# Performance work log

Measured on AMD Instinct MI355X. Metric: run time of the kernel, lower is better.

## Reference

```python
import jax, jax.numpy as jnp
import numpy as np

TOP_K = 2


def setup_inputs() -> dict:
    key = jax.random.key(0)
    ks = jax.random.split(key, 5)
    B, S, H, F, E = 1, 2048, 1024, 3584, 8
    scale_h = 1.0 / np.sqrt(H)
    scale_f = 1.0 / np.sqrt(F)
    return {
        "hidden_states": jax.random.normal(ks[0], (B, S, H), dtype=jnp.float32),
        "gate_w": jax.random.normal(ks[1], (E, H), dtype=jnp.float32) * scale_h,
        "w1": jax.random.normal(ks[2], (E, H, F), dtype=jnp.float32) * scale_h,
        "w3": jax.random.normal(ks[3], (E, H, F), dtype=jnp.float32) * scale_h,
        "w2": jax.random.normal(ks[4], (E, F, H), dtype=jnp.float32) * scale_f,
    }


def reference(hidden_states, gate_w, w1, w2, w3):
    B, S, H = hidden_states.shape
    E = gate_w.shape[0]
    x = hidden_states.reshape(-1, H)  # [T, H]
    # Router: logits -> fp32 softmax -> top-k -> renormalize
    router_logits = x @ gate_w.T  # [T, E]
    probs = jax.nn.softmax(router_logits.astype(jnp.float32), axis=-1)
    top_w, top_idx = jax.lax.top_k(probs, TOP_K)  # [T, K]
    top_w = top_w / jnp.sum(top_w, axis=-1, keepdims=True)
    top_w = top_w.astype(x.dtype)
    # Dense combine weights [T, E]: routing weight if expert selected else 0
    combine = jnp.sum(jax.nn.one_hot(top_idx, E, dtype=x.dtype) * top_w[..., None], axis=1)
    # Per-expert SwiGLU FFN, weighted-summed (loop over small fixed E)
    out = jnp.zeros_like(x)
    for e in range(E):
        h = jax.nn.silu(x @ w1[e]) * (x @ w3[e])  # [T, F]
        out = out + (h @ w2[e]) * combine[:, e:e + 1]
    return out.reshape(B, S, H), router_logits
```

## Files before the change

kernel.cpp:

```cpp
#include <hip/hip_runtime.h>
#include <cstdint>
#include <cstddef>

#define Tt 2048
#define Hh 1024
#define Ff 3584
#define Ee 8
#define ROWS_CAP 5120
#define MAXT 40

#define OFF_CTRL   0u
#define OFF_TOKE   4096u
#define OFF_TOKW   (4096u + 16384u)
#define OFF_ROWMAP 65536u
#define OFF_ROWW   98304u
#define OFF_XG     262144ull
#define OFF_G      10747904ull
#define OFF_W1T    47448064ull
#define OFF_W3T    106168320ull
#define OFF_W2T    164888576ull

typedef __attribute__((ext_vector_type(8))) short bf16x8;
typedef __attribute__((ext_vector_type(4))) float f32x4;

__device__ __forceinline__ unsigned short f2bf(float f) {
  unsigned int u = __float_as_uint(f);
  u += 0x7fffu + ((u >> 16) & 1u);
  return (unsigned short)(u >> 16);
}

__device__ __forceinline__ unsigned pkbf(float a, float b) {
  unsigned r;
  asm("v_cvt_pk_bf16_f32 %0, %1, %2" : "=v"(r) : "v"(a), "v"(b));
  return r;
}

__device__ __forceinline__ void gload_lds16(const void* g, void* l) {
  auto gp = (const __attribute__((address_space(1))) char*)(uintptr_t)g;
  auto lp = (__attribute__((address_space(3))) char*)(uintptr_t)l;
  __builtin_amdgcn_global_load_lds(gp, lp, 16, 0, 0);
}

__device__ __forceinline__ bf16x8 frg(const char* lds, int row, int gc) {
  return *(const bf16x8*)(lds + row * 64 + ((gc ^ ((row >> 1) & 3)) * 16));
}

__device__ __forceinline__ void tc_tile(const float* __restrict__ src,
                                        unsigned short* __restrict__ dst,
                                        int R, int C, int r0g, int c0,
                                        char* sT, int t) {
  const int col4 = (t & 15) * 4, rb = (t >> 4) * 8;
  float4 v[8];
#pragma unroll
  for (int i = 0; i < 8; ++i)
    v[i] = *(const float4*)(src + (size_t)(r0g + rb + i) * C + c0 + col4);
#pragma unroll
  for (int j = 0; j < 4; ++j) {
    int c = col4 + j;
    int M = (((c & 7) ^ ((c >> 3) & 7)) << 4);
    uint4 q;
    q.x = pkbf(((const float*)&v[0])[j], ((const float*)&v[1])[j]);
    q.y = pkbf(((const float*)&v[2])[j], ((const float*)&v[3])[j]);
    q.z = pkbf(((const float*)&v[4])[j], ((const float*)&v[5])[j]);
    q.w = pkbf(((const float*)&v[6])[j], ((const float*)&v[7])[j]);
    *(uint4*)(sT + c * 256 + ((rb * 2) ^ M)) = q;
  }
  __syncthreads();
  const int oc = t >> 2, part = t & 3;
  const int M = (((oc & 7) ^ ((oc >> 3) & 7)) << 4);
#pragma unroll
  for (int i = 0; i < 4; ++i) {
    uint4 q = *(const uint4*)(sT + oc * 256 + ((i * 64 + part * 16) ^ M));
    *(uint4*)(dst + (size_t)(c0 + oc) * R + r0g + i * 32 + part * 8) = q;
  }
}

__global__ __launch_bounds__(256) void router_tc1(
    const float* __restrict__ x, const float* __restrict__ gw,
    float* __restrict__ logits_out, int* __restrict__ tok_e,
    float* __restrict__ tok_w, int* __restrict__ ctrl,
    const float* __restrict__ w1, unsigned short* __restrict__ w1T) {
  __shared__ alignas(16) char sT[16384];
  if (blockIdx.x >= 512) {
    int b = blockIdx.x - 512;
    int e = b / 448, rem = b % 448;
    int tr = rem / 56, tcc = rem % 56;
    tc_tile(w1 + (size_t)e * Hh * Ff, w1T + (size_t)e * Hh * Ff,
            Hh, Ff, tr * 128, tcc * 64, sT, threadIdx.x);
    return;
  }
  const int lane = threadIdx.x & 63;
  const int t = blockIdx.x * 4 + (threadIdx.x >> 6);
  const float4* xp = (const float4*)(x + (size_t)t * Hh + lane * 16);
  float4 x0 = xp[0], x1 = xp[1], x2 = xp[2], x3 = xp[3];
  float lg[Ee];
#pragma unroll
  for (int e = 0; e < Ee; ++e) {
    const float4* gp = (const float4*)(gw + e * Hh + lane * 16);
    float4 g0 = gp[0], g1 = gp[1], g2 = gp[2], g3 = gp[3];
    float s = x0.x*g0.x + x0.y*g0.y + x0.z*g0.z + x0.w*g0.w
            + x1.x*g1.x + x1.y*g1.y + x1.z*g1.z + x1.w*g1.w
            + x2.x*g2.x + x2.y*g2.y + x2.z*g2.z + x2.w*g2.w
            + x3.x*g3.x + x3.y*g3.y + x3.z*g3.z + x3.w*g3.w;
#pragma unroll
    for (int o = 32; o; o >>= 1) s += __shfl_xor(s, o);
    lg[e] = s;
  }
  if (lane == 0) {
    float m = lg[0];
#pragma unroll
    for (int e = 1; e < Ee; ++e) m = fmaxf(m, lg[e]);
    float p[Ee];
#pragma unroll
    for (int e = 0; e < Ee; ++e) p[e] = expf(lg[e] - m);
    int a0 = 0;
#pragma unroll
    for (int e = 1; e < Ee; ++e) if (p[e] > p[a0]) a0 = e;
    int a1 = (a0 == 0) ? 1 : 0;
#pragma unroll
    for (int e = 0; e < Ee; ++e) if (e != a0 && p[e] > p[a1]) a1 = e;
    float rs = p[a0] + p[a1];
    float w0 = p[a0] / rs, w1v = p[a1] / rs;
#pragma unroll
    for (int e = 0; e < Ee; ++e) logits_out[(size_t)t * Ee + e] = lg[e];
    tok_e[t * 2] = a0; tok_e[t * 2 + 1] = a1;
    tok_w[t * 2] = w0; tok_w[t * 2 + 1] = w1v;
    atomicAdd(&ctrl[a0], 1); atomicAdd(&ctrl[a1], 1);
  }
}

__global__ void offsets_kernel(int* ctrl) {
  if (threadIdx.x == 0) {
    int acc = 0;
    for (int e = 0; e < Ee; ++e) {
      ctrl[16 + e] = acc;
      acc += ((ctrl[e] + 127) >> 7) << 7;
    }
    ctrl[16 + Ee] = acc;
    int idx = 0;
    for (int e = 0; e < Ee; ++e) {
      int nt = (ctrl[e] + 127) >> 7;
      for (int m = 0; m < nt && idx < MAXT; ++m) {
        ctrl[32 + 2 * idx] = e;
        ctrl[33 + 2 * idx] = ctrl[16 + e] + m * 128;
        ++idx;
      }
    }
    for (; idx < MAXT; ++idx) { ctrl[32 + 2 * idx] = 0; ctrl[33 + 2 * idx] = -1; }
  }
}

__global__ __launch_bounds__(512) void assign_kernel(
    int* ctrl, const int* __restrict__ tok_e, const float* __restrict__ tok_w,
    int* __restrict__ rowmap, float* __restrict__ roww) {
  int i = blockIdx.x * 512 + threadIdx.x;
  if (i < 2 * Tt) {
    int e = tok_e[i];
    int pos = atomicAdd(&ctrl[8 + e], 1);
    int r = ctrl[16 + e] + pos;
    rowmap[r] = i >> 1;
    roww[r] = tok_w[i];
  }
  if (i < Ee * 128) {
    int e = i >> 7, pd = i & 127;
    int o = ctrl[16 + e], o1 = ctrl[16 + e + 1], c = ctrl[e];
    int r = o + c + pd;
    if (r < o1) { rowmap[r] = -1; roww[r] = 0.f; }
  }
}

__global__ __launch_bounds__(256) void gather_tc3(
    const float* __restrict__ x, const int* __restrict__ ctrl,
    const int* __restrict__ rowmap, unsigned short* __restrict__ Xg,
    const float* __restrict__ w3, unsigned short* __restrict__ w3T) {
  __shared__ alignas(16) char sT[16384];
  if (blockIdx.x >= 2560) {
    int b = blockIdx.x - 2560;
    int e = b / 448, rem = b % 448;
    int tr = rem / 56, tcc = rem % 56;
    tc_tile(w3 + (size_t)e * Hh * Ff, w3T + (size_t)e * Hh * Ff,
            Hh, Ff, tr * 128, tcc * 64, sT, threadIdx.x);
    return;
  }
  int r = blockIdx.x * 2 + (threadIdx.x >> 7);
  int j = threadIdx.x & 127;
  if (r >= ctrl[16 + Ee]) return;
  int t = rowmap[r];
  uint4 v = make_uint4(0u, 0u, 0u, 0u);
  if (t >= 0) {
    const float4* xp = (const float4*)(x + (size_t)t * Hh + j * 8);
    float4 a = xp[0], b = xp[1];
    v.x = (unsigned)f2bf(a.x) | ((unsigned)f2bf(a.y) << 16);
    v.y = (unsigned)f2bf(a.z) | ((unsigned)f2bf(a.w) << 16);
    v.z = (unsigned)f2bf(b.x) | ((unsigned)f2bf(b.y) << 16);
    v.w = (unsigned)f2bf(b.z) | ((unsigned)f2bf(b.w) << 16);
  }
  *(uint4*)(Xg + (size_t)r * Hh + j * 8) = v;
}

__global__ __launch_bounds__(512, 4) void h13_tc2(
    const unsigned short* __restrict__ Xg, const unsigned short* __restrict__ w1T,
    const unsigned short* __restrict__ w3T, const int* __restrict__ ctrl,
    unsigned short* __restrict__ G,
    const float* __restrict__ w2, unsigned short* __restrict__ w2T) {
  __shared__ alignas(16) char sLDS[49152];
  int lin = blockIdx.y * 28 + blockIdx.x;
  if (lin >= 1120) {
    int idx = lin - 1120;
    int s = threadIdx.x >> 8;
    int tile = idx * 2 + s;
    int e = tile / 448, rem = tile % 448;
    int tr = rem / 16, tcc = rem % 16;
    tc_tile(w2 + (size_t)e * Ff * Hh, w2T + (size_t)e * Ff * Hh,
            Ff, Hh, tr * 128, tcc * 64, sLDS + s * 16384, threadIdx.x & 255);
    return;
  }
  char* sA  = sLDS;
  char* sB1 = sLDS + 16384;
  char* sB3 = sLDS + 32768;
  int wg = (lin & 7) * 140 + (lin >> 3);
  int ft = wg % 40, bx = wg / 40;
  const int e = ctrl[32 + 2 * ft];
  const int row0 = ctrl[33 + 2 * ft];
  if (row0 < 0) return;
  const int n0 = bx * 128;
  const int tid = threadIdx.x, lane = tid & 63, wv = tid >> 6;
  const int wr = wv >> 2, wc = wv & 3;
  const unsigned short* w1e = w1T + (size_t)e * Ff * Hh;
  const unsigned short* w3e = w3T + (size_t)e * Ff * Hh;
  f32x4 acc1[4][2] = {};
  f32x4 acc3[4][2] = {};
  const int srow = wv * 16 + (lane >> 2);
  const int sgc = (lane & 3) ^ ((lane >> 3) & 3);
  const unsigned short* gA  = Xg  + (size_t)(row0 + srow) * Hh + sgc * 8;
  const unsigned short* gB1 = w1e + (size_t)(n0 + srow) * Hh + sgc * 8;
  const unsigned short* gB3 = w3e + (size_t)(n0 + srow) * Hh + sgc * 8;

  gload_lds16(gA,  sA  + wv * 1024);
  gload_lds16(gB1, sB1 + wv * 1024);
  gload_lds16(gB3, sB3 + wv * 1024);
  __syncthreads();

  for (int it = 0; it < 32; ++it) {
    const int cur = it & 1;
    if (it < 31) {
      const size_t ko = (size_t)(it + 1) * 32;
      gload_lds16(gA + ko,  sA  + (cur ^ 1) * 8192 + wv * 1024);
      gload_lds16(gB1 + ko, sB1 + (cur ^ 1) * 8192 + wv * 1024);
      gload_lds16(gB3 + ko, sB3 + (cur ^ 1) * 8192 + wv * 1024);
    }
    const int gc = lane >> 4;
    bf16x8 af[4];
#pragma unroll
    for (int mi = 0; mi < 4; ++mi)
      af[mi] = frg(sA + cur * 8192, wr * 64 + mi * 16 + (lane & 15), gc);
    __builtin_amdgcn_s_setprio(1);
#pragma unroll
    for (int ni = 0; ni < 2; ++ni) {
      bf16x8 b1 = frg(sB1 + cur * 8192, wc * 32 + ni * 16 + (lane & 15), gc);
      bf16x8 b3 = frg(sB3 + cur * 8192, wc * 32 + ni * 16 + (lane & 15), gc);
#pragma unroll
      for (int mi = 0; mi < 4; ++mi) {
        acc1[mi][ni] = __builtin_amdgcn_mfma_f32_16x16x32_bf16(af[mi], b1, acc1[mi][ni], 0, 0, 0);
        acc3[mi][ni] = __builtin_amdgcn_mfma_f32_16x16x32_bf16(af[mi], b3, acc3[mi][ni], 0, 0, 0);
      }
    }
    __builtin_amdgcn_s_setprio(0);
    __syncthreads();
  }
  const int rb = wr * 64 + 4 * (lane >> 4), cb = wc * 32 + (lane & 15);
#pragma unroll
  for (int mi = 0; mi < 4; ++mi)
#pragma unroll
    for (int ni = 0; ni < 2; ++ni)
#pragma unroll
      for (int r = 0; r < 4; ++r) {
        float h1 = acc1[mi][ni][r], h3 = acc3[mi][ni][r];
        float gv = h1 / (1.f + __expf(-h1)) * h3;
        G[(size_t)(row0 + rb + mi * 16 + r) * Ff + n0 + cb + ni * 16] = f2bf(gv);
      }
}

__global__ __launch_bounds__(512, 4) void ffn2_gemm(
    const unsigned short* __restrict__ G, const unsigned short* __restrict__ w2T,
    const int* __restrict__ ctrl, const int* __restrict__ rowmap,
    const float* __restrict__ roww, float* __restrict__ out) {
  __shared__ alignas(16) char sA[2][8192], sB[2][8192];
  int lin = (blockIdx.z * MAXT + blockIdx.y) * 8 + blockIdx.x;
  int wg = (lin & 7) * 160 + (lin >> 3);
  int ft = wg % 40, q = wg / 40;
  int bx = q & 7, ks = q >> 3;
  const int e = ctrl[32 + 2 * ft];
  const int row0 = ctrl[33 + 2 * ft];
  if (row0 < 0) return;
  const int n0 = bx * 128;
  const int kb = ks * (Ff / 4);
  const int tid = threadIdx.x, lane = tid & 63, wv = tid >> 6;
  const int wr = wv >> 2, wc = wv & 3;
  const unsigned short* w2e = w2T + (size_t)e * Ff * Hh;
  f32x4 acc[4][2] = {};
  const int srow = wv * 16 + (lane >> 2);
  const int sgc = (lane & 3) ^ ((lane >> 3) & 3);
  const unsigned short* gA = G   + (size_t)(row0 + srow) * Ff + kb + sgc * 8;
  const unsigned short* gB = w2e + (size_t)(n0 + srow) * Ff + kb + sgc * 8;

  gload_lds16(gA, sA[0] + wv * 1024);
  gload_lds16(gB, sB[0] + wv * 1024);
  __syncthreads();

  const int NT = 28;
  for (int it = 0; it < NT; ++it) {
    const int cur = it & 1;
    if (it < NT - 1) {
      const size_t ko = (size_t)(it + 1) * 32;
      gload_lds16(gA + ko, sA[cur ^ 1] + wv * 1024);
      gload_lds16(gB + ko, sB[cur ^ 1] + wv * 1024);
    }
    const int gc = lane >> 4;
    bf16x8 af[4];
#pragma unroll
    for (int mi = 0; mi < 4; ++mi)
      af[mi] = frg(sA[cur], wr * 64 + mi * 16 + (lane & 15), gc);
    __builtin_amdgcn_s_setprio(1);
#pragma unroll
    for (int ni = 0; ni < 2; ++ni) {
      bf16x8 b = frg(sB[cur], wc * 32 + ni * 16 + (lane & 15), gc);
#pragma unroll
      for (int mi = 0; mi < 4; ++mi)
        acc[mi][ni] = __builtin_amdgcn_mfma_f32_16x16x32_bf16(af[mi], b, acc[mi][ni], 0, 0, 0);
    }
    __builtin_amdgcn_s_setprio(0);
    __syncthreads();
  }
  const int rb = wr * 64 + 4 * (lane >> 4), cb = wc * 32 + (lane & 15);
#pragma unroll
  for (int mi = 0; mi < 4; ++mi)
#pragma unroll
    for (int r = 0; r < 4; ++r) {
      int grow = row0 + rb + mi * 16 + r;
      int t = rowmap[grow];
      if (t < 0) continue;
      float wgt = roww[grow];
#pragma unroll
      for (int ni = 0; ni < 2; ++ni)
        atomicAdd(&out[(size_t)t * Hh + n0 + cb + ni * 16], wgt * acc[mi][ni][r]);
    }
}

extern "C" void kernel_launch(void* const* d_in, const int* in_sizes, int n_in,
                              void* d_out, int out_size, void* d_ws, size_t ws_size,
                              hipStream_t stream) {
  const float* x  = (const float*)d_in[0];
  const float* gw = (const float*)d_in[1];
  const float* w1 = (const float*)d_in[2];
  const float* w3 = (const float*)d_in[3];
  const float* w2 = (const float*)d_in[4];
  float* out = (float*)d_out;
  float* logits = out + (size_t)Tt * Hh;
  char* ws = (char*)d_ws;
  int* ctrl = (int*)(ws + OFF_CTRL);
  int* tok_e = (int*)(ws + OFF_TOKE);
  float* tok_w = (float*)(ws + OFF_TOKW);
  int* rowmap = (int*)(ws + OFF_ROWMAP);
  float* roww = (float*)(ws + OFF_ROWW);
  unsigned short* Xg  = (unsigned short*)(ws + OFF_XG);
  unsigned short* G   = (unsigned short*)(ws + OFF_G);
  unsigned short* w1T = (unsigned short*)(ws + OFF_W1T);
  unsigned short* w3T = (unsigned short*)(ws + OFF_W3T);
  unsigned short* w2T = (unsigned short*)(ws + OFF_W2T);

  hipMemsetAsync(ctrl, 0, 512, stream);
  hipMemsetAsync(out, 0, (size_t)Tt * Hh * sizeof(float), stream);
  router_tc1<<<512 + 3584, 256, 0, stream>>>(x, gw, logits, tok_e, tok_w, ctrl, w1, w1T);
  offsets_kernel<<<1, 64, 0, stream>>>(ctrl);
  assign_kernel<<<8, 512, 0, stream>>>(ctrl, tok_e, tok_w, rowmap, roww);
  gather_tc3<<<2560 + 3584, 256, 0, stream>>>(x, ctrl, rowmap, Xg, w3, w3T);
  h13_tc2<<<dim3(28, 104), 512, 0, stream>>>(Xg, w1T, w3T, ctrl, G, w2, w2T);
  ffn2_gemm<<<dim3(8, MAXT, 4), 512, 0, stream>>>(G, w2T, ctrl, rowmap, roww, out);
}
```

Measured before the change: 343.6 us.

## Interleave w1/w3 into one B matrix, enlarge h13 tiles, triple-buffer GEMM loads

```diff
diff --git a/kernel.cpp b/kernel.cpp
--- a/kernel.cpp
+++ b/kernel.cpp
@@ -6,8 +6,9 @@
 #define Hh 1024
 #define Ff 3584
 #define Ee 8
-#define ROWS_CAP 5120
+#define NP 7168
 #define MAXT 40
+#define MAXT2 24
 
 #define OFF_CTRL   0u
 #define OFF_TOKE   4096u
@@ -15,10 +16,9 @@
 #define OFF_ROWMAP 65536u
 #define OFF_ROWW   98304u
 #define OFF_XG     262144ull
-#define OFF_G      10747904ull
-#define OFF_W1T    47448064ull
-#define OFF_W3T    106168320ull
-#define OFF_W2T    164888576ull
+#define OFF_G      11272192ull
+#define OFF_W13T   47972352ull
+#define OFF_W2T    165412864ull
 
 typedef __attribute__((ext_vector_type(8))) short bf16x8;
 typedef __attribute__((ext_vector_type(4))) float f32x4;
@@ -48,7 +48,7 @@
 __device__ __forceinline__ void tc_tile(const float* __restrict__ src,
                                         unsigned short* __restrict__ dst,
                                         int R, int C, int r0g, int c0,
-                                        char* sT, int t) {
+                                        char* sT, int t, int mode) {
   const int col4 = (t & 15) * 4, rb = (t >> 4) * 8;
   float4 v[8];
 #pragma unroll
@@ -68,10 +68,12 @@
   __syncthreads();
   const int oc = t >> 2, part = t & 3;
   const int M = (((oc & 7) ^ ((oc >> 3) & 7)) << 4);
+  int cg = c0 + oc;
+  int orow = (mode == 0) ? cg : (((cg >> 4) << 5) + (cg & 15) + (mode == 2 ? 16 : 0));
 #pragma unroll
   for (int i = 0; i < 4; ++i) {
     uint4 q = *(const uint4*)(sT + oc * 256 + ((i * 64 + part * 16) ^ M));
-    *(uint4*)(dst + (size_t)(c0 + oc) * R + r0g + i * 32 + part * 8) = q;
+    *(uint4*)(dst + (size_t)orow * R + r0g + i * 32 + part * 8) = q;
   }
 }
 
@@ -79,14 +81,14 @@
     const float* __restrict__ x, const float* __restrict__ gw,
     float* __restrict__ logits_out, int* __restrict__ tok_e,
     float* __restrict__ tok_w, int* __restrict__ ctrl,
-    const float* __restrict__ w1, unsigned short* __restrict__ w1T) {
+    const float* __restrict__ w1, unsigned short* __restrict__ w13T) {
   __shared__ alignas(16) char sT[16384];
   if (blockIdx.x >= 512) {
     int b = blockIdx.x - 512;
     int e = b / 448, rem = b % 448;
     int tr = rem / 56, tcc = rem % 56;
-    tc_tile(w1 + (size_t)e * Hh * Ff, w1T + (size_t)e * Hh * Ff,
-            Hh, Ff, tr * 128, tcc * 64, sT, threadIdx.x);
+    tc_tile(w1 + (size_t)e * Hh * Ff, w13T + (size_t)e * NP * Hh,
+            Hh, Ff, tr * 128, tcc * 64, sT, threadIdx.x, 1);
     return;
   }
   const int lane = threadIdx.x & 63;
@@ -147,6 +149,18 @@
       }
     }
     for (; idx < MAXT; ++idx) { ctrl[32 + 2 * idx] = 0; ctrl[33 + 2 * idx] = -1; }
+    int idx2 = 0;
+    for (int e = 0; e < Ee; ++e) {
+      int sz = ((ctrl[e] + 127) >> 7) << 7;
+      int nt = (sz + 255) >> 8;
+      for (int m = 0; m < nt && idx2 < MAXT2; ++m) {
+        ctrl[128 + 3 * idx2] = e;
+        ctrl[129 + 3 * idx2] = ctrl[16 + e] + m * 256;
+        ctrl[130 + 3 * idx2] = ctrl[16 + e] + sz;
+        ++idx2;
+      }
+    }
+    for (; idx2 < MAXT2; ++idx2) { ctrl[128 + 3 * idx2] = 0; ctrl[129 + 3 * idx2] = -1; ctrl[130 + 3 * idx2] = 0; }
   }
 }
 
@@ -172,14 +186,14 @@
 __global__ __launch_bounds__(256) void gather_tc3(
     const float* __restrict__ x, const int* __restrict__ ctrl,
     const int* __restrict__ rowmap, unsigned short* __restrict__ Xg,
-    const float* __restrict__ w3, unsigned short* __restrict__ w3T) {
+    const float* __restrict__ w3, unsigned short* __restrict__ w13T) {
   __shared__ alignas(16) char sT[16384];
   if (blockIdx.x >= 2560) {
     int b = blockIdx.x - 2560;
     int e = b / 448, rem = b % 448;
     int tr = rem / 56, tcc = rem % 56;
-    tc_tile(w3 + (size_t)e * Hh * Ff, w3T + (size_t)e * Hh * Ff,
-            Hh, Ff, tr * 128, tcc * 64, sT, threadIdx.x);
+    tc_tile(w3 + (size_t)e * Hh * Ff, w13T + (size_t)e * NP * Hh,
+            Hh, Ff, tr * 128, tcc * 64, sT, threadIdx.x, 2);
     return;
   }
   int r = blockIdx.x * 2 + (threadIdx.x >> 7);
@@ -198,94 +212,102 @@
   *(uint4*)(Xg + (size_t)r * Hh + j * 8) = v;
 }
 
-__global__ __launch_bounds__(512, 4) void h13_tc2(
-    const unsigned short* __restrict__ Xg, const unsigned short* __restrict__ w1T,
-    const unsigned short* __restrict__ w3T, const int* __restrict__ ctrl,
-    unsigned short* __restrict__ G,
+__global__ __launch_bounds__(1024, 4) void h13_tc2(
+    const unsigned short* __restrict__ Xg, const unsigned short* __restrict__ w13T,
+    const int* __restrict__ ctrl, unsigned short* __restrict__ G,
     const float* __restrict__ w2, unsigned short* __restrict__ w2T) {
-  __shared__ alignas(16) char sLDS[49152];
+  __shared__ alignas(16) char sLDS[98304];
   int lin = blockIdx.y * 28 + blockIdx.x;
-  if (lin >= 1120) {
-    int idx = lin - 1120;
+  if (lin >= 672) {
+    int idx = lin - 672;
     int s = threadIdx.x >> 8;
-    int tile = idx * 2 + s;
+    int tile = idx * 4 + s;
     int e = tile / 448, rem = tile % 448;
     int tr = rem / 16, tcc = rem % 16;
     tc_tile(w2 + (size_t)e * Ff * Hh, w2T + (size_t)e * Ff * Hh,
-            Ff, Hh, tr * 128, tcc * 64, sLDS + s * 16384, threadIdx.x & 255);
+            Ff, Hh, tr * 128, tcc * 64, sLDS + s * 16384, threadIdx.x & 255, 0);
     return;
   }
-  char* sA  = sLDS;
-  char* sB1 = sLDS + 16384;
-  char* sB3 = sLDS + 32768;
-  int wg = (lin & 7) * 140 + (lin >> 3);
-  int ft = wg % 40, bx = wg / 40;
-  const int e = ctrl[32 + 2 * ft];
-  const int row0 = ctrl[33 + 2 * ft];
+  int wg = (lin & 7) * 84 + (lin >> 3);
+  int ft = wg % 24, bx = wg / 24;
+  const int e = ctrl[128 + 3 * ft];
+  const int row0 = ctrl[129 + 3 * ft];
+  const int off1 = ctrl[130 + 3 * ft];
   if (row0 < 0) return;
-  const int n0 = bx * 128;
+  const int n0 = bx * 256;
   const int tid = threadIdx.x, lane = tid & 63, wv = tid >> 6;
   const int wr = wv >> 2, wc = wv & 3;
-  const unsigned short* w1e = w1T + (size_t)e * Ff * Hh;
-  const unsigned short* w3e = w3T + (size_t)e * Ff * Hh;
-  f32x4 acc1[4][2] = {};
-  f32x4 acc3[4][2] = {};
+  const unsigned short* wB = w13T + (size_t)e * NP * Hh;
+  f32x4 acc[4][4] = {};
   const int srow = wv * 16 + (lane >> 2);
   const int sgc = (lane & 3) ^ ((lane >> 3) & 3);
-  const unsigned short* gA  = Xg  + (size_t)(row0 + srow) * Hh + sgc * 8;
-  const unsigned short* gB1 = w1e + (size_t)(n0 + srow) * Hh + sgc * 8;
-  const unsigned short* gB3 = w3e + (size_t)(n0 + srow) * Hh + sgc * 8;
-
-  gload_lds16(gA,  sA  + wv * 1024);
-  gload_lds16(gB1, sB1 + wv * 1024);
-  gload_lds16(gB3, sB3 + wv * 1024);
-  __syncthreads();
+  const unsigned short* gA = Xg + (size_t)(row0 + srow) * Hh + sgc * 8;
+  const unsigned short* gB = wB + (size_t)(n0 + srow) * Hh + sgc * 8;
+  char *cA = sLDS,          *nA = sLDS + 16384, *xA = sLDS + 32768;
+  char *cB = sLDS + 49152,  *nB = sLDS + 65536, *xB = sLDS + 81920;
+
+  gload_lds16(gA, cA + wv * 1024);
+  gload_lds16(gB, cB + wv * 1024);
+  __builtin_amdgcn_sched_barrier(0);
+  gload_lds16(gA + 32, nA + wv * 1024);
+  gload_lds16(gB + 32, nB + wv * 1024);
+  asm volatile("s_waitcnt vmcnt(0) lgkmcnt(0)" ::: "memory");
+  __builtin_amdgcn_s_barrier();
+  __builtin_amdgcn_sched_barrier(0);
 
   for (int it = 0; it < 32; ++it) {
-    const int cur = it & 1;
+    if (it < 30) {
+      gload_lds16(gA + (size_t)(it + 2) * 32, xA + wv * 1024);
+      gload_lds16(gB + (size_t)(it + 2) * 32, xB + wv * 1024);
+    }
+    __builtin_amdgcn_sched_barrier(0);
+    {
+      const int gc = lane >> 4;
+      bf16x8 af[4];
+#pragma unroll
+      for (int mi = 0; mi < 4; ++mi)
+        af[mi] = frg(cA, wr * 64 + mi * 16 + (lane & 15), gc);
+      __builtin_amdgcn_s_setprio(1);
+#pragma unroll
+      for (int ni = 0; ni < 4; ++ni) {
+        bf16x8 b = frg(cB, wc * 64 + ni * 16 + (lane & 15), gc);
+#pragma unroll
+        for (int mi = 0; mi < 4; ++mi)
+          acc[mi][ni] = __builtin_amdgcn_mfma_f32_16x16x32_bf16(af[mi], b, acc[mi][ni], 0, 0, 0);
+      }
+      __builtin_amdgcn_s_setprio(0);
+    }
     if (it < 31) {
-      const size_t ko = (size_t)(it + 1) * 32;
-      gload_lds16(gA + ko,  sA  + (cur ^ 1) * 8192 + wv * 1024);
-      gload_lds16(gB1 + ko, sB1 + (cur ^ 1) * 8192 + wv * 1024);
-      gload_lds16(gB3 + ko, sB3 + (cur ^ 1) * 8192 + wv * 1024);
-    }
-    const int gc = lane >> 4;
-    bf16x8 af[4];
-#pragma unroll
-    for (int mi = 0; mi < 4; ++mi)
-      af[mi] = frg(sA + cur * 8192, wr * 64 + mi * 16 + (lane & 15), gc);
-    __builtin_amdgcn_s_setprio(1);
-#pragma unroll
-    for (int ni = 0; ni < 2; ++ni) {
-      bf16x8 b1 = frg(sB1 + cur * 8192, wc * 32 + ni * 16 + (lane & 15), gc);
-      bf16x8 b3 = frg(sB3 + cur * 8192, wc * 32 + ni * 16 + (lane & 15), gc);
-#pragma unroll
-      for (int mi = 0; mi < 4; ++mi) {
-        acc1[mi][ni] = __builtin_amdgcn_mfma_f32_16x16x32_bf16(af[mi], b1, acc1[mi][ni], 0, 0, 0);
-        acc3[mi][ni] = __builtin_amdgcn_mfma_f32_16x16x32_bf16(af[mi], b3, acc3[mi][ni], 0, 0, 0);
+      if (it < 30) asm volatile("s_waitcnt vmcnt(2) lgkmcnt(0)" ::: "memory");
+      else         asm volatile("s_waitcnt vmcnt(0) lgkmcnt(0)" ::: "memory");
+      __builtin_amdgcn_s_barrier();
+      __builtin_amdgcn_sched_barrier(0);
+    }
+    { char* t_ = cA; cA = nA; nA = xA; xA = t_;
+      t_ = cB; cB = nB; nB = xB; xB = t_; }
+  }
+  const int rb = wr * 64 + 4 * (lane >> 4);
+  const int f0 = (n0 >> 1) + wc * 32 + (lane & 15);
+#pragma unroll
+  for (int mi = 0; mi < 4; ++mi)
+#pragma unroll
+    for (int r = 0; r < 4; ++r) {
+      int grow = row0 + rb + mi * 16 + r;
+      if (grow >= off1) continue;
+#pragma unroll
+      for (int nq = 0; nq < 2; ++nq) {
+        float h1 = acc[mi][2 * nq][r], h3 = acc[mi][2 * nq + 1][r];
+        float gv = h1 / (1.f + __expf(-h1)) * h3;
+        G[(size_t)grow * Ff + f0 + nq * 16] = f2bf(gv);
       }
     }
-    __builtin_amdgcn_s_setprio(0);
-    __syncthreads();
-  }
-  const int rb = wr * 64 + 4 * (lane >> 4), cb = wc * 32 + (lane & 15);
-#pragma unroll
-  for (int mi = 0; mi < 4; ++mi)
-#pragma unroll
-    for (int ni = 0; ni < 2; ++ni)
-#pragma unroll
-      for (int r = 0; r < 4; ++r) {
-        float h1 = acc1[mi][ni][r], h3 = acc3[mi][ni][r];
-        float gv = h1 / (1.f + __expf(-h1)) * h3;
-        G[(size_t)(row0 + rb + mi * 16 + r) * Ff + n0 + cb + ni * 16] = f2bf(gv);
-      }
 }
 
 __global__ __launch_bounds__(512, 4) void ffn2_gemm(
     const unsigned short* __restrict__ G, const unsigned short* __restrict__ w2T,
     const int* __restrict__ ctrl, const int* __restrict__ rowmap,
     const float* __restrict__ roww, float* __restrict__ out) {
-  __shared__ alignas(16) char sA[2][8192], sB[2][8192];
+  __shared__ alignas(16) char sLDS[49152];
   int lin = (blockIdx.z * MAXT + blockIdx.y) * 8 + blockIdx.x;
   int wg = (lin & 7) * 160 + (lin >> 3);
   int ft = wg % 40, q = wg / 40;
@@ -303,34 +325,49 @@
   const int sgc = (lane & 3) ^ ((lane >> 3) & 3);
   const unsigned short* gA = G   + (size_t)(row0 + srow) * Ff + kb + sgc * 8;
   const unsigned short* gB = w2e + (size_t)(n0 + srow) * Ff + kb + sgc * 8;
-
-  gload_lds16(gA, sA[0] + wv * 1024);
-  gload_lds16(gB, sB[0] + wv * 1024);
-  __syncthreads();
+  char *cA = sLDS,         *nA = sLDS + 8192,  *xA = sLDS + 16384;
+  char *cB = sLDS + 24576, *nB = sLDS + 32768, *xB = sLDS + 40960;
+
+  gload_lds16(gA, cA + wv * 1024);
+  gload_lds16(gB, cB + wv * 1024);
+  __builtin_amdgcn_sched_barrier(0);
+  gload_lds16(gA + 32, nA + wv * 1024);
+  gload_lds16(gB + 32, nB + wv * 1024);
+  asm volatile("s_waitcnt vmcnt(0) lgkmcnt(0)" ::: "memory");
+  __builtin_amdgcn_s_barrier();
+  __builtin_amdgcn_sched_barrier(0);
 
   const int NT = 28;
   for (int it = 0; it < NT; ++it) {
-    const int cur = it & 1;
+    if (it < NT - 2) {
+      gload_lds16(gA + (size_t)(it + 2) * 32, xA + wv * 1024);
+      gload_lds16(gB + (size_t)(it + 2) * 32, xB + wv * 1024);
+    }
+    __builtin_amdgcn_sched_barrier(0);
+    {
+      const int gc = lane >> 4;
+      bf16x8 af[4];
+#pragma unroll
+      for (int mi = 0; mi < 4; ++mi)
+        af[mi] = frg(cA, wr * 64 + mi * 16 + (lane & 15), gc);
+      __builtin_amdgcn_s_setprio(1);
+#pragma unroll
+      for (int ni = 0; ni < 2; ++ni) {
+        bf16x8 b = frg(cB, wc * 32 + ni * 16 + (lane & 15), gc);
+#pragma unroll
+        for (int mi = 0; mi < 4; ++mi)
+          acc[mi][ni] = __builtin_amdgcn_mfma_f32_16x16x32_bf16(af[mi], b, acc[mi][ni], 0, 0, 0);
+      }
+      __builtin_amdgcn_s_setprio(0);
+    }
     if (it < NT - 1) {
-      const size_t ko = (size_t)(it + 1) * 32;
-      gload_lds16(gA + ko, sA[cur ^ 1] + wv * 1024);
-      gload_lds16(gB + ko, sB[cur ^ 1] + wv * 1024);
-    }
-    const int gc = lane >> 4;
-    bf16x8 af[4];
-#pragma unroll
-    for (int mi = 0; mi < 4; ++mi)
-      af[mi] = frg(sA[cur], wr * 64 + mi * 16 + (lane & 15), gc);
-    __builtin_amdgcn_s_setprio(1);
-#pragma unroll
-    for (int ni = 0; ni < 2; ++ni) {
-      bf16x8 b = frg(sB[cur], wc * 32 + ni * 16 + (lane & 15), gc);
-#pragma unroll
-      for (int mi = 0; mi < 4; ++mi)
-        acc[mi][ni] = __builtin_amdgcn_mfma_f32_16x16x32_bf16(af[mi], b, acc[mi][ni], 0, 0, 0);
-    }
-    __builtin_amdgcn_s_setprio(0);
-    __syncthreads();
+      if (it < NT - 2) asm volatile("s_waitcnt vmcnt(2) lgkmcnt(0)" ::: "memory");
+      else             asm volatile("s_waitcnt vmcnt(0) lgkmcnt(0)" ::: "memory");
+      __builtin_amdgcn_s_barrier();
+      __builtin_amdgcn_sched_barrier(0);
+    }
+    { char* t_ = cA; cA = nA; nA = xA; xA = t_;
+      t_ = cB; cB = nB; nB = xB; xB = t_; }
   }
   const int rb = wr * 64 + 4 * (lane >> 4), cb = wc * 32 + (lane & 15);
 #pragma unroll
@@ -363,18 +400,17 @@
   float* tok_w = (float*)(ws + OFF_TOKW);
   int* rowmap = (int*)(ws + OFF_ROWMAP);
   float* roww = (float*)(ws + OFF_ROWW);
-  unsigned short* Xg  = (unsigned short*)(ws + OFF_XG);
-  unsigned short* G   = (unsigned short*)(ws + OFF_G);
-  unsigned short* w1T = (unsigned short*)(ws + OFF_W1T);
-  unsigned short* w3T = (unsigned short*)(ws + OFF_W3T);
-  unsigned short* w2T = (unsigned short*)(ws + OFF_W2T);
-
-  hipMemsetAsync(ctrl, 0, 512, stream);
+  unsigned short* Xg   = (unsigned short*)(ws + OFF_XG);
+  unsigned short* G    = (unsigned short*)(ws + OFF_G);
+  unsigned short* w13T = (unsigned short*)(ws + OFF_W13T);
+  unsigned short* w2T  = (unsigned short*)(ws + OFF_W2T);
+
+  hipMemsetAsync(ctrl, 0, 1024, stream);
   hipMemsetAsync(out, 0, (size_t)Tt * Hh * sizeof(float), stream);
-  router_tc1<<<512 + 3584, 256, 0, stream>>>(x, gw, logits, tok_e, tok_w, ctrl, w1, w1T);
+  router_tc1<<<512 + 3584, 256, 0, stream>>>(x, gw, logits, tok_e, tok_w, ctrl, w1, w13T);
   offsets_kernel<<<1, 64, 0, stream>>>(ctrl);
   assign_kernel<<<8, 512, 0, stream>>>(ctrl, tok_e, tok_w, rowmap, roww);
-  gather_tc3<<<2560 + 3584, 256, 0, stream>>>(x, ctrl, rowmap, Xg, w3, w3T);
-  h13_tc2<<<dim3(28, 104), 512, 0, stream>>>(Xg, w1T, w3T, ctrl, G, w2, w2T);
+  gather_tc3<<<2560 + 3584, 256, 0, stream>>>(x, ctrl, rowmap, Xg, w3, w13T);
+  h13_tc2<<<dim3(28, 56), 1024, 0, stream>>>(Xg, w13T, ctrl, G, w2, w2T);
   ffn2_gemm<<<dim3(8, MAXT, 4), 512, 0, stream>>>(G, w2T, ctrl, rowmap, roww, out);
 }
```

New measurement: 350.9 us. 1.02x slower.
